# Kernel tuning notes

Measured on AMD Instinct MI355X. Metric: run time of the kernel, lower is better.

The kernel has to match this reference:

```python
import jax, jax.numpy as jnp
import numpy as np

B, S, H, D = 2, 2048, 16, 128
HID = H * D
THETA = 10000.0
SCALE = 1.0 / np.sqrt(D)


def setup_inputs() -> dict:
    key = jax.random.key(0)
    k1, k2, k3 = jax.random.split(key, 3)
    x = jax.random.normal(k1, (B, S, HID), dtype=jnp.float32)
    w_qkv = jax.random.normal(k2, (3 * HID, HID), dtype=jnp.float32) * 0.02
    w_o = jax.random.normal(k3, (HID, HID), dtype=jnp.float32) * 0.02
    return {"x": x, "w_qkv": w_qkv, "w_o": w_o}


def _rope_cos_sin(seq_len, dim, dtype):
    inv_freq = 1.0 / (THETA ** (jnp.arange(0, dim, 2, dtype=jnp.float32) / dim))
    pos = jnp.arange(seq_len, dtype=jnp.float32)
    freqs = pos[:, None] * inv_freq[None, :]          # (S, D/2)
    emb = jnp.concatenate([freqs, freqs], axis=-1)    # (S, D)
    return jnp.cos(emb).astype(dtype), jnp.sin(emb).astype(dtype)


def _rotate_half(t):
    t1, t2 = jnp.split(t, 2, axis=-1)
    return jnp.concatenate([-t2, t1], axis=-1)


def reference(x, w_qkv, w_o):
    b, s, _ = x.shape
    qkv = jnp.einsum('bsh,oh->bso', x, w_qkv)                 # (B,S,3*HID)
    qkv = qkv.reshape(b, s, 3, H, D).transpose(2, 0, 3, 1, 4)  # (3,B,H,S,D)
    q, k, v = qkv[0], qkv[1], qkv[2]
    cos, sin = _rope_cos_sin(s, D, x.dtype)                    # (S,D)
    q = q * cos + _rotate_half(q) * sin
    k = k * cos + _rotate_half(k) * sin
    scores = jnp.einsum('bhqd,bhkd->bhqk', q, k) * SCALE       # (B,H,S,S)
    causal = jnp.triu(jnp.ones((s, s), dtype=bool), k=1)
    scores = jnp.where(causal[None, None], -jnp.inf, scores)
    attn = jax.nn.softmax(scores.astype(jnp.float32), axis=-1).astype(q.dtype)
    out = jnp.einsum('bhqk,bhkd->bhqd', attn, v)               # (B,H,S,D)
    out = out.transpose(0, 2, 1, 3).reshape(b, s, HID)
    return jnp.einsum('bsh,oh->bso', out, w_o)
```

## Files before the change

kernel.cpp:

```cpp
#include <hip/hip_runtime.h>
#include <hip/hip_bf16.h>

typedef unsigned short u16;
typedef unsigned long long u64;
typedef u16 us8 __attribute__((ext_vector_type(8)));
typedef __bf16 bf8_t __attribute__((ext_vector_type(8)));
typedef float f32x4 __attribute__((ext_vector_type(4)));

__device__ __forceinline__ float b2f(u16 u) {
    return __uint_as_float(((unsigned int)u) << 16);
}
__device__ __forceinline__ u16 f2b(float f) {
    union { __hip_bfloat16 h; u16 u; } v;
    v.h = __float2bfloat16(f);
    return v.u;
}
__device__ __forceinline__ f32x4 mfma16(bf8_t a, bf8_t b, f32x4 c) {
    return __builtin_amdgcn_mfma_f32_16x16x32_bf16(a, b, c, 0, 0, 0);
}
__device__ __forceinline__ void gload_lds16(const u16* g, u16* lds_base) {
    __builtin_amdgcn_global_load_lds((const __attribute__((address_space(1))) unsigned int*)g,
                                     (__attribute__((address_space(3))) unsigned int*)lds_base,
                                     16, 0, 0);
}

__global__ __launch_bounds__(256) void f32_to_bf16(const float* __restrict__ src,
                                                   u16* __restrict__ dst, int n8) {
    int idx = blockIdx.x * 256 + threadIdx.x;
    if (idx >= n8) return;
    float4 f0 = ((const float4*)src)[idx * 2];
    float4 f1 = ((const float4*)src)[idx * 2 + 1];
    us8 o;
    o[0] = f2b(f0.x); o[1] = f2b(f0.y); o[2] = f2b(f0.z); o[3] = f2b(f0.w);
    o[4] = f2b(f1.x); o[5] = f2b(f1.y); o[6] = f2b(f1.z); o[7] = f2b(f1.w);
    ((us8*)dst)[idx] = o;
}

template<int STORE_F32>
__global__ __launch_bounds__(256) void gemm_mfma_bt(const u16* __restrict__ A, const u16* __restrict__ B,
                                                    void* __restrict__ Cout, int M, int N, int K, int ldc) {
    __shared__ u16 Alds[128 * 32];
    __shared__ u16 Blds[128 * 32];
    const int tid = threadIdx.x;
    const int lane = tid & 63, wave = tid >> 6;
    const int lm = lane & 15, lq = lane >> 4;
    const int wm = wave >> 1, wn = wave & 1;
    const int m0 = blockIdx.y * 128, n0 = blockIdx.x * 128;
    const int srow = lane >> 2;
    const int scol = (lane & 3) * 8;

    f32x4 acc[4][4] = {};

    for (int k0 = 0; k0 < K; k0 += 32) {
#pragma unroll
        for (int p = 0; p < 2; p++) {
            int rbase = wave * 16 + p * 64;
            gload_lds16(A + (size_t)(m0 + rbase + srow) * K + k0 + scol, &Alds[rbase * 32]);
            gload_lds16(B + (size_t)(n0 + rbase + srow) * K + k0 + scol, &Blds[rbase * 32]);
        }
        __syncthreads();
        bf8_t af[4], bf[4];
#pragma unroll
        for (int mb = 0; mb < 4; mb++)
            af[mb] = *(const bf8_t*)&Alds[(wm * 64 + mb * 16 + lm) * 32 + lq * 8];
#pragma unroll
        for (int nb = 0; nb < 4; nb++)
            bf[nb] = *(const bf8_t*)&Blds[(wn * 64 + nb * 16 + lm) * 32 + lq * 8];
#pragma unroll
        for (int mb = 0; mb < 4; mb++)
#pragma unroll
            for (int nb = 0; nb < 4; nb++)
                acc[mb][nb] = mfma16(af[mb], bf[nb], acc[mb][nb]);
        __syncthreads();
    }
#pragma unroll
    for (int mb = 0; mb < 4; mb++)
#pragma unroll
        for (int nb = 0; nb < 4; nb++)
#pragma unroll
            for (int r = 0; r < 4; r++) {
                int row = m0 + wm * 64 + mb * 16 + lq * 4 + r;
                int col = n0 + wn * 64 + nb * 16 + lm;
                if (STORE_F32)
                    ((float*)Cout)[(size_t)row * ldc + col] = acc[mb][nb][r];
                else
                    ((u16*)Cout)[(size_t)row * ldc + col] = f2b(acc[mb][nb][r]);
            }
}

__global__ __launch_bounds__(256) void rope_vt(u16* __restrict__ qkv, u16* __restrict__ VT) {
    __shared__ u16 T[64 * 136];
    const int tid = threadIdx.x;
    const int s0 = blockIdx.x * 64;
    const int bh = blockIdx.y;
    const int b = bh >> 4, h = bh & 15;
#pragma unroll
    for (int p = 0; p < 4; p++) {
        int sl = p * 16 + (tid >> 4);
        int d0 = (tid & 15) * 8;
        *(us8*)&T[sl * 136 + d0] =
            *(const us8*)(qkv + ((size_t)(b * 2048 + s0 + sl)) * 6144 + 4096 + h * 128 + d0);
    }
#pragma unroll
    for (int p = 0; p < 2; p++) {
        int task = p * 256 + tid;
        int sl = task >> 3;
        int jg = task & 7;
        size_t base = ((size_t)(b * 2048 + s0 + sl)) * 6144 + h * 128 + jg * 8;
        us8 qlo = *(const us8*)(qkv + base);
        us8 qhi = *(const us8*)(qkv + base + 64);
        us8 klo = *(const us8*)(qkv + base + 2048);
        us8 khi = *(const us8*)(qkv + base + 2048 + 64);
        us8 oql, oqh, okl, okh;
        float s = (float)(s0 + sl);
#pragma unroll
        for (int e = 0; e < 8; e++) {
            int j = jg * 8 + e;
            float inv = __expf((float)j * (-9.210340371976184f / 64.f));
            float ang = s * inv;
            float sn, c;
            __sincosf(ang, &sn, &c);
            float q1 = b2f(qlo[e]), q2 = b2f(qhi[e]);
            oql[e] = f2b(q1 * c - q2 * sn);
            oqh[e] = f2b(q2 * c + q1 * sn);
            float k1 = b2f(klo[e]), k2 = b2f(khi[e]);
            okl[e] = f2b(k1 * c - k2 * sn);
            okh[e] = f2b(k2 * c + k1 * sn);
        }
        *(us8*)(qkv + base) = oql;
        *(us8*)(qkv + base + 64) = oqh;
        *(us8*)(qkv + base + 2048) = okl;
        *(us8*)(qkv + base + 2048 + 64) = okh;
    }
    __syncthreads();
#pragma unroll
    for (int p = 0; p < 4; p++) {
        int idx = p * 256 + tid;
        int d = idx & 127;
        int sg = idx >> 7;
        us8 v;
#pragma unroll
        for (int i = 0; i < 8; i++) v[i] = T[(sg * 8 + i) * 136 + d];
        *(us8*)&VT[((size_t)bh * 128 + d) * 2048 + s0 + sg * 8] = v;
    }
}

#define ATT_SCALE 0.08838834764831845f

__global__ __launch_bounds__(256, 2) void attn_flash(const u16* __restrict__ qkv, const u16* __restrict__ VT,
                                                     u16* __restrict__ AO) {
    const int bid = blockIdx.x;
    const int swz = (bid & 7) * 64 + (bid >> 3);
    const int bh = swz >> 4;
    const int pair = swz & 15;
    const int b = bh >> 4, h = bh & 15;
    const int tid = threadIdx.x, lane = tid & 63, wave = tid >> 6;
    const int lm = lane & 15, lq = lane >> 4;

    const int jq0 = 31 - pair;
    const int jq1 = pair;
    const int ktmax = jq0;

    __shared__ u16 Kt[64 * 136];
    __shared__ u16 Vt[128 * 72];

    bf8_t qf[2][4];
#pragma unroll
    for (int qg = 0; qg < 2; qg++) {
        const int jqv = qg ? jq1 : jq0;
        const u16* Qrow = qkv + ((size_t)(b * 2048 + jqv * 64 + wave * 16 + lm)) * 6144 + h * 128;
#pragma unroll
        for (int ks = 0; ks < 4; ks++)
            qf[qg][ks] = *(const bf8_t*)(Qrow + ks * 32 + lq * 8);
    }

    f32x4 Of[2][8] = {};
    float mrun[2] = {-3.0e38f, -3.0e38f}, lrun[2] = {0.f, 0.f};

    const u16* Kbase = qkv + (size_t)b * 2048 * 6144 + 2048 + h * 128;
    const u16* VTbase = VT + (size_t)bh * 128 * 2048;

    const int krow = tid >> 4;
    const int kcol = (tid & 15) * 8;
    const int vrow = tid >> 3;
    const int vcol = (tid & 7) * 8;

    us8 kreg[4], vreg[4];
#pragma unroll
    for (int p = 0; p < 4; p++) {
        kreg[p] = *(const us8*)(Kbase + (size_t)(p * 16 + krow) * 6144 + kcol);
        vreg[p] = *(const us8*)(VTbase + (size_t)(p * 32 + vrow) * 2048 + vcol);
    }

    for (int kt = 0; kt <= ktmax; kt++) {
        __syncthreads();
#pragma unroll
        for (int p = 0; p < 4; p++) {
            *(us8*)&Kt[(p * 16 + krow) * 136 + kcol] = kreg[p];
            *(us8*)&Vt[(p * 32 + vrow) * 72 + vcol] = vreg[p];
        }
        __syncthreads();
        {
            int kn = (kt + 1 <= ktmax ? kt + 1 : ktmax) * 64;
#pragma unroll
            for (int p = 0; p < 4; p++) {
                kreg[p] = *(const us8*)(Kbase + (size_t)(kn + p * 16 + krow) * 6144 + kcol);
                vreg[p] = *(const us8*)(VTbase + (size_t)(p * 32 + vrow) * 2048 + kn + vcol);
            }
        }

        const bool act1 = (kt <= jq1);
        u64 pk[2][4];
#pragma unroll
        for (int qg = 0; qg < 2; qg++) {
            if (qg == 0 || act1) {
                const int jqv = qg ? jq1 : jq0;
                float sv[4][4];
#pragma unroll
                for (int nb = 0; nb < 4; nb++) {
                    f32x4 a = {};
#pragma unroll
                    for (int ks = 0; ks < 4; ks++) {
                        bf8_t kf = *(const bf8_t*)&Kt[(nb * 16 + lm) * 136 + ks * 32 + lq * 8];
                        a = mfma16(kf, qf[qg][ks], a);
                    }
#pragma unroll
                    for (int r = 0; r < 4; r++) sv[nb][r] = a[r] * ATT_SCALE;
                }
                if (kt == jqv) {
                    int qglob = jqv * 64 + wave * 16 + lm;
#pragma unroll
                    for (int nb = 0; nb < 4; nb++)
#pragma unroll
                        for (int r = 0; r < 4; r++)
                            if (kt * 64 + nb * 16 + lq * 4 + r > qglob) sv[nb][r] = -3.0e38f;
                }
                float mx = -3.0e38f;
#pragma unroll
                for (int nb = 0; nb < 4; nb++)
#pragma unroll
                    for (int r = 0; r < 4; r++) mx = fmaxf(mx, sv[nb][r]);
                mx = fmaxf(mx, __shfl_xor(mx, 16, 64));
                mx = fmaxf(mx, __shfl_xor(mx, 32, 64));
                float mnew = fmaxf(mrun[qg], mx);
                float a_ = __expf(mrun[qg] - mnew);
                float rs = 0.f;
#pragma unroll
                for (int nb = 0; nb < 4; nb++) {
                    float e0 = __expf(sv[nb][0] - mnew), e1 = __expf(sv[nb][1] - mnew);
                    float e2 = __expf(sv[nb][2] - mnew), e3 = __expf(sv[nb][3] - mnew);
                    rs += (e0 + e1) + (e2 + e3);
                    unsigned int lo = (unsigned int)f2b(e0) | ((unsigned int)f2b(e1) << 16);
                    unsigned int hi = (unsigned int)f2b(e2) | ((unsigned int)f2b(e3) << 16);
                    pk[qg][nb] = (u64)lo | ((u64)hi << 32);
                }
                rs += __shfl_xor(rs, 16, 64);
                rs += __shfl_xor(rs, 32, 64);
                lrun[qg] = lrun[qg] * a_ + rs;
                mrun[qg] = mnew;
#pragma unroll
                for (int db = 0; db < 8; db++)
#pragma unroll
                    for (int r = 0; r < 4; r++) Of[qg][db][r] *= a_;
            }
        }

        const int slo = ((lq & 1) * 2) * 16 + lm;
        const int shi = slo + 16;
        const bool sel = (lq >> 1) != 0;
#pragma unroll
        for (int kk = 0; kk < 2; kk++) {
            union { u64 v[2]; bf8_t f; } pf[2];
#pragma unroll
            for (int qg = 0; qg < 2; qg++) {
                if (qg == 0 || act1) {
                    u64 lo0 = __shfl(pk[qg][2 * kk + 0], slo, 64);
                    u64 lo1 = __shfl(pk[qg][2 * kk + 1], slo, 64);
                    u64 hi0 = __shfl(pk[qg][2 * kk + 0], shi, 64);
                    u64 hi1 = __shfl(pk[qg][2 * kk + 1], shi, 64);
                    pf[qg].v[0] = sel ? lo1 : lo0;
                    pf[qg].v[1] = sel ? hi1 : hi0;
                }
            }
#pragma unroll
            for (int db = 0; db < 8; db++) {
                bf8_t vf = *(const bf8_t*)&Vt[(db * 16 + lm) * 72 + kk * 32 + lq * 8];
                Of[0][db] = mfma16(vf, pf[0].f, Of[0][db]);
                if (act1) Of[1][db] = mfma16(vf, pf[1].f, Of[1][db]);
            }
        }
    }
#pragma unroll
    for (int qg = 0; qg < 2; qg++) {
        const int jqv = qg ? jq1 : jq0;
        float invl = 1.f / lrun[qg];
        size_t rowbase = (size_t)(b * 2048 + jqv * 64 + wave * 16 + lm) * 2048 + h * 128;
#pragma unroll
        for (int db = 0; db < 8; db++) {
            ushort4 o;
            o.x = f2b(Of[qg][db][0] * invl);
            o.y = f2b(Of[qg][db][1] * invl);
            o.z = f2b(Of[qg][db][2] * invl);
            o.w = f2b(Of[qg][db][3] * invl);
            *(ushort4*)(AO + rowbase + db * 16 + lq * 4) = o;
        }
    }
}

extern "C" void kernel_launch(void* const* d_in, const int* in_sizes, int n_in,
                              void* d_out, int out_size, void* d_ws, size_t ws_size,
                              hipStream_t stream) {
    const float* x     = (const float*)d_in[0];
    const float* w_qkv = (const float*)d_in[1];
    const float* w_o   = (const float*)d_in[2];
    float* out = (float*)d_out;
    u16* ws = (u16*)d_ws;

    u16* qkvb  = ws;
    u16* VT    = ws + 25165824;
    u16* AO    = ws + 33554432;
    u16* xb    = ws + 41943040;
    u16* wqkvb = ws + 50331648;
    u16* wob   = ws + 62914560;

    f32_to_bf16<<<4096, 256, 0, stream>>>(x, xb, 1048576);
    f32_to_bf16<<<6144, 256, 0, stream>>>(w_qkv, wqkvb, 1572864);
    f32_to_bf16<<<2048, 256, 0, stream>>>(w_o, wob, 524288);
    gemm_mfma_bt<0><<<dim3(48, 32), 256, 0, stream>>>(xb, wqkvb, qkvb, 4096, 6144, 2048, 6144);
    rope_vt<<<dim3(32, 32), 256, 0, stream>>>(qkvb, VT);
    attn_flash<<<dim3(512), 256, 0, stream>>>(qkvb, VT, AO);
    gemm_mfma_bt<1><<<dim3(16, 32), 256, 0, stream>>>(AO, wob, out, 4096, 2048, 2048, 2048);
}
```

Before: 419.3 us.

## Replace GEMM with 256x128 double-buffered pipelined MFMA kernel

Replaces the simple 128x128, K=32 single-buffered GEMM with a 512-thread 256x128 tile kernel using K=64 double-buffered LDS, direct global-to-LDS loads interleaved with MFMA quadrants, an XOR swizzle against LDS bank conflicts, and an XCD-aware block remap. The aim is to hide global load latency behind compute and raise arithmetic intensity in both projection GEMMs. It hardcodes K=2048 and M tile count 16, which removes generality, and it relies on hand-placed barriers and waitcnts for correctness.

```diff
diff --git a/kernel.cpp b/kernel.cpp
--- a/kernel.cpp
+++ b/kernel.cpp
@@ -36,55 +36,144 @@
     ((us8*)dst)[idx] = o;
 }
 
-template<int STORE_F32>
-__global__ __launch_bounds__(256) void gemm_mfma_bt(const u16* __restrict__ A, const u16* __restrict__ B,
-                                                    void* __restrict__ Cout, int M, int N, int K, int ldc) {
-    __shared__ u16 Alds[128 * 32];
-    __shared__ u16 Blds[128 * 32];
+#define BARX() __builtin_amdgcn_s_barrier()
+#define LGKM0() do { asm volatile("s_waitcnt lgkmcnt(0)" ::: "memory"); \
+                     __builtin_amdgcn_sched_barrier(0); } while (0)
+#define VM6()   do { asm volatile("s_waitcnt vmcnt(6)" ::: "memory"); \
+                     __builtin_amdgcn_sched_barrier(0); } while (0)
+
+template<int SF32>
+__global__ __launch_bounds__(512, 2) void gemm256(const u16* __restrict__ A,
+                                                  const u16* __restrict__ B,
+                                                  void* __restrict__ Cout, int ldc) {
+    __shared__ u16 LA[2][2][128 * 64];
+    __shared__ u16 LB[2][128 * 64];
+
     const int tid = threadIdx.x;
-    const int lane = tid & 63, wave = tid >> 6;
+    const int w = tid >> 6, lane = tid & 63;
     const int lm = lane & 15, lq = lane >> 4;
-    const int wm = wave >> 1, wn = wave & 1;
-    const int m0 = blockIdx.y * 128, n0 = blockIdx.x * 128;
-    const int srow = lane >> 2;
-    const int scol = (lane & 3) * 8;
-
+    const int wm = w >> 1, wn = w & 1;
+
+    const int bid = blockIdx.x;
+    const int nper = gridDim.x >> 3;
+    const int wg = (bid & 7) * nper + (bid >> 3);
+    const int mt = wg & 15, nt = wg >> 4;
+    const int m0 = mt * 256, n0 = nt * 128;
+
+    const int lp = lane ^ ((lane & 32) >> 4);
+    const int srow = lp >> 3;
+    const int scol = (lp & 7) * 8;
+
+    const u16* Abase = A + (size_t)(m0 + srow) * 2048 + scol;
+    const u16* Bbase = B + (size_t)(n0 + srow) * 2048 + scol;
+
+#define STAGE_A(c, h, kt) do { \
+    int _k0 = (kt) * 64; \
+    _Pragma("unroll") \
+    for (int i = 0; i < 2; i++) { \
+        int R = w * 2 + i; \
+        gload_lds16(Abase + (size_t)((h) * 128 + R * 8) * 2048 + _k0, &LA[c][h][R * 512]); \
+    } } while (0)
+
+#define STAGE_B(c, kt) do { \
+    int _k0 = (kt) * 64; \
+    _Pragma("unroll") \
+    for (int i = 0; i < 2; i++) { \
+        int R = w * 2 + i; \
+        gload_lds16(Bbase + (size_t)(R * 8) * 2048 + _k0, &LB[c][R * 512]); \
+    } } while (0)
+
+    bf8_t af[4][2], bfr[4][2];
     f32x4 acc[4][4] = {};
-
-    for (int k0 = 0; k0 < K; k0 += 32) {
-#pragma unroll
-        for (int p = 0; p < 2; p++) {
-            int rbase = wave * 16 + p * 64;
-            gload_lds16(A + (size_t)(m0 + rbase + srow) * K + k0 + scol, &Alds[rbase * 32]);
-            gload_lds16(B + (size_t)(n0 + rbase + srow) * K + k0 + scol, &Blds[rbase * 32]);
-        }
-        __syncthreads();
-        bf8_t af[4], bf[4];
-#pragma unroll
-        for (int mb = 0; mb < 4; mb++)
-            af[mb] = *(const bf8_t*)&Alds[(wm * 64 + mb * 16 + lm) * 32 + lq * 8];
-#pragma unroll
-        for (int nb = 0; nb < 4; nb++)
-            bf[nb] = *(const bf8_t*)&Blds[(wn * 64 + nb * 16 + lm) * 32 + lq * 8];
-#pragma unroll
-        for (int mb = 0; mb < 4; mb++)
-#pragma unroll
-            for (int nb = 0; nb < 4; nb++)
-                acc[mb][nb] = mfma16(af[mb], bf[nb], acc[mb][nb]);
-        __syncthreads();
-    }
-#pragma unroll
-    for (int mb = 0; mb < 4; mb++)
-#pragma unroll
-        for (int nb = 0; nb < 4; nb++)
+    const int ahalf = wm >> 1;
+    const int arbase = (wm & 1) * 64;
+    const int brbase = wn * 64;
+
+#define READ_FRAGS(c) do { \
+    _Pragma("unroll") \
+    for (int m = 0; m < 4; m++) { \
+        int rl = arbase + m * 16 + lm; \
+        _Pragma("unroll") \
+        for (int ks = 0; ks < 2; ks++) { \
+            int o = rl * 128 + ks * 64 + lq * 16; \
+            o ^= ((o >> 9) & 1) << 5; \
+            af[m][ks] = *(const bf8_t*)((const char*)&LA[c][ahalf][0] + o); \
+        } \
+    } \
+    _Pragma("unroll") \
+    for (int n = 0; n < 4; n++) { \
+        int rl = brbase + n * 16 + lm; \
+        _Pragma("unroll") \
+        for (int ks = 0; ks < 2; ks++) { \
+            int o = rl * 128 + ks * 64 + lq * 16; \
+            o ^= ((o >> 9) & 1) << 5; \
+            bfr[n][ks] = *(const bf8_t*)((const char*)&LB[c][0] + o); \
+        } \
+    } } while (0)
+
+#define QUAD(mh, nh) do { \
+    __builtin_amdgcn_s_setprio(1); \
+    _Pragma("unroll") \
+    for (int m = 0; m < 2; m++) \
+    _Pragma("unroll") \
+    for (int n = 0; n < 2; n++) \
+    _Pragma("unroll") \
+    for (int ks = 0; ks < 2; ks++) \
+        acc[(mh)*2+m][(nh)*2+n] = \
+            mfma16(af[(mh)*2+m][ks], bfr[(nh)*2+n][ks], acc[(mh)*2+m][(nh)*2+n]); \
+    __builtin_amdgcn_s_setprio(0); \
+    } while (0)
+
+    STAGE_B(0, 0); STAGE_A(0, 0, 0); STAGE_A(0, 1, 0);
+    STAGE_B(1, 1); STAGE_A(1, 0, 1); STAGE_A(1, 1, 1);
+    VM6();
+    BARX();
+
+    for (int it = 0; it < 16; it++) {
+        const int t2 = (2 * it + 2 < 32) ? 2 * it + 2 : 31;
+        const int t3 = (2 * it + 3 < 32) ? 2 * it + 3 : 31;
+        READ_FRAGS(0);
+        BARX(); LGKM0();
+        QUAD(0, 0);
+        BARX();
+        STAGE_B(0, t2);
+        QUAD(0, 1);
+        BARX();
+        STAGE_A(0, 0, t2);
+        QUAD(1, 0);
+        BARX();
+        STAGE_A(0, 1, t2);
+        QUAD(1, 1);
+        VM6();
+        BARX();
+        READ_FRAGS(1);
+        BARX(); LGKM0();
+        QUAD(0, 0);
+        BARX();
+        STAGE_B(1, t3);
+        QUAD(0, 1);
+        BARX();
+        STAGE_A(1, 0, t3);
+        QUAD(1, 0);
+        BARX();
+        STAGE_A(1, 1, t3);
+        QUAD(1, 1);
+        VM6();
+        BARX();
+    }
+
+#pragma unroll
+    for (int m = 0; m < 4; m++)
+#pragma unroll
+        for (int n = 0; n < 4; n++)
 #pragma unroll
             for (int r = 0; r < 4; r++) {
-                int row = m0 + wm * 64 + mb * 16 + lq * 4 + r;
-                int col = n0 + wn * 64 + nb * 16 + lm;
-                if (STORE_F32)
-                    ((float*)Cout)[(size_t)row * ldc + col] = acc[mb][nb][r];
+                int row = m0 + wm * 64 + m * 16 + lq * 4 + r;
+                int col = n0 + wn * 64 + n * 16 + lm;
+                if (SF32)
+                    ((float*)Cout)[(size_t)row * ldc + col] = acc[m][n][r];
                 else
-                    ((u16*)Cout)[(size_t)row * ldc + col] = f2b(acc[mb][nb][r]);
+                    ((u16*)Cout)[(size_t)row * ldc + col] = f2b(acc[m][n][r]);
             }
 }
 
@@ -326,8 +415,8 @@
     f32_to_bf16<<<4096, 256, 0, stream>>>(x, xb, 1048576);
     f32_to_bf16<<<6144, 256, 0, stream>>>(w_qkv, wqkvb, 1572864);
     f32_to_bf16<<<2048, 256, 0, stream>>>(w_o, wob, 524288);
-    gemm_mfma_bt<0><<<dim3(48, 32), 256, 0, stream>>>(xb, wqkvb, qkvb, 4096, 6144, 2048, 6144);
+    gemm256<0><<<768, 512, 0, stream>>>(xb, wqkvb, qkvb, 6144);
     rope_vt<<<dim3(32, 32), 256, 0, stream>>>(qkvb, VT);
     attn_flash<<<dim3(512), 256, 0, stream>>>(qkvb, VT, AO);
-    gemm_mfma_bt<1><<<dim3(16, 32), 256, 0, stream>>>(AO, wob, out, 4096, 2048, 2048, 2048);
-}
+    gemm256<1><<<256, 512, 0, stream>>>(AO, wob, out, 2048);
+}
```

Result: faster. 403.5 us (-3.8%).
